# Performance work log

Hardware: AMD Instinct MI355X
Metric: run time of the kernel (lower is better)

Reference implementation:

```python
import jax, jax.numpy as jnp
import numpy as np

DIM = 768
HEADS = 12
SCALE = DIM ** -0.5  # NOTE: module scales by full dim, not head dim


def setup_inputs() -> dict:
    key = jax.random.key(0)
    ks = jax.random.split(key, 5)
    B, N, C = 8, 1024, DIM
    x = jax.random.normal(ks[0], (B, N, C), dtype=jnp.float32)
    W_qkv = jax.random.normal(ks[1], (C, 3 * C), dtype=jnp.float32) * (C ** -0.5)
    b_qkv = jnp.zeros((3 * C,), dtype=jnp.float32)
    W_out = jax.random.normal(ks[2], (C, C), dtype=jnp.float32) * (C ** -0.5)
    b_out = jnp.zeros((C,), dtype=jnp.float32)
    return {"x": x, "W_qkv": W_qkv, "b_qkv": b_qkv, "W_out": W_out, "b_out": b_out}


def reference(x, W_qkv, b_qkv, W_out, b_out) -> jnp.ndarray:
    B, N, C = x.shape
    H, D = HEADS, C // HEADS
    qkv = x @ W_qkv + b_qkv                       # [B, N, 3C]
    q, k, v = jnp.split(qkv, 3, axis=-1)
    # [B, N, C] -> [B, H, N, D]
    q = q.reshape(B, N, H, D).transpose(0, 2, 1, 3)
    k = k.reshape(B, N, H, D).transpose(0, 2, 1, 3)
    v = v.reshape(B, N, H, D).transpose(0, 2, 1, 3)
    attn = jnp.einsum("bhnd,bhmd->bhnm", q, k) * SCALE
    attn = jax.nn.softmax(attn, axis=-1)
    out = jnp.einsum("bhnm,bhmd->bhnd", attn, v)   # [B, H, N, D]
    out = out.transpose(0, 2, 1, 3).reshape(B, N, C)
    return out @ W_out + b_out
```

## Files before the change

kernel.cpp:

```cpp
#include <hip/hip_runtime.h>
#include <hip/hip_bf16.h>

typedef __attribute__((ext_vector_type(4))) float f32x4;
typedef __attribute__((ext_vector_type(4))) unsigned u32x4;
typedef __attribute__((ext_vector_type(8))) short bf16x8;

#define QSCALE  (0.03608439182435161f * 1.44269504088896f)

__device__ __forceinline__ unsigned short f2bf(float f) {
    union { float f; unsigned u; } v; v.f = f;
    return (unsigned short)((v.u + 0x7FFFu + ((v.u >> 16) & 1u)) >> 16);
}

__device__ __forceinline__ float fast_exp2(float x) {
#if __has_builtin(__builtin_amdgcn_exp2f)
    return __builtin_amdgcn_exp2f(x);
#else
    return exp2f(x);
#endif
}

__device__ __forceinline__ void gload_lds16(const void* g, void* l) {
    __builtin_amdgcn_global_load_lds(
        (const __attribute__((address_space(1))) unsigned int*)g,
        (__attribute__((address_space(3))) unsigned int*)l, 16, 0, 0);
}

__global__ __launch_bounds__(256) void prep_kernel(
    const float* __restrict__ X, unsigned short* __restrict__ Xb,
    const float* __restrict__ Wqkv, unsigned short* __restrict__ WqkvT,
    const float* __restrict__ Wout, unsigned short* __restrict__ WoutT)
{
    __shared__ unsigned short T[64][68];
    const int bid = blockIdx.x, t = threadIdx.x;

    if (bid < 3072) {
        const int i = bid * 256 + t;
        f32x4 a = *(const f32x4*)(X + (size_t)i * 8);
        f32x4 b = *(const f32x4*)(X + (size_t)i * 8 + 4);
        bf16x8 w;
#pragma unroll
        for (int j = 0; j < 4; ++j) { w[j] = (short)f2bf(a[j]); w[4 + j] = (short)f2bf(b[j]); }
        *(bf16x8*)(Xb + (size_t)i * 8) = w;
        return;
    }

    const float* W; unsigned short* WT; int C, bx, by;
    if (bid < 3504) { W = Wqkv; WT = WqkvT; C = 2304; const int x = bid - 3072; bx = x % 36; by = x / 36; }
    else            { W = Wout; WT = WoutT; C = 768;  const int x = bid - 3504; bx = x % 12; by = x / 12; }
    const int R = 768;
    const int r0 = by * 64, c0 = bx * 64;
    {
        const int lr = t >> 4, lc = (t & 15) * 4;
#pragma unroll
        for (int p = 0; p < 4; ++p) {
            const float* s = W + (size_t)(r0 + lr + p * 16) * C + c0 + lc;
            f32x4 v = *(const f32x4*)s;
            unsigned short* d = &T[lr + p * 16][lc];
            d[0] = f2bf(v[0]); d[1] = f2bf(v[1]); d[2] = f2bf(v[2]); d[3] = f2bf(v[3]);
        }
    }
    __syncthreads();
    {
        const int oc = t >> 3, j0 = (t & 7) * 8;
#pragma unroll
        for (int p = 0; p < 2; ++p) {
            const int c = oc + p * 32;
            bf16x8 v;
#pragma unroll
            for (int j = 0; j < 8; ++j) v[j] = (short)T[j0 + j][c];
            *(bf16x8*)(WT + (size_t)(c0 + c) * R + r0 + j0) = v;
        }
    }
}

__global__ __launch_bounds__(256) void qkv_gemm_kernel(
    const unsigned short* __restrict__ Xb, const unsigned short* __restrict__ WT,
    const float* __restrict__ bias,
    unsigned short* __restrict__ Qw, unsigned short* __restrict__ Kw,
    unsigned short* __restrict__ VTw)
{
    __shared__ unsigned short SMEM[64 * 136 + 64];
    unsigned short* Alds = SMEM;
    unsigned short* Blds = SMEM + 128 * 32;

    const int t = threadIdx.x;
    const int lane = t & 63, wave = t >> 6;
    const int l15 = lane & 15, l4 = lane >> 4;
    const int m0 = blockIdx.x * 128, n0 = blockIdx.y * 64;
    const int wr = wave >> 1, wc = wave & 1;

    f32x4 acc[4][2];
#pragma unroll
    for (int m = 0; m < 4; ++m)
#pragma unroll
        for (int n = 0; n < 2; ++n) acc[m][n] = (f32x4){0.f, 0.f, 0.f, 0.f};

    for (int k0 = 0; k0 < 768; k0 += 32) {
#pragma unroll
        for (int c = 0; c < 2; ++c) {
            const int o = wave * 1024 + lane * 16 + c * 4096;
            const int row = o >> 6, cb = o & 63;
            gload_lds16((const char*)(Xb + (size_t)(m0 + row) * 768 + k0) + cb,
                        (char*)Alds + wave * 1024 + c * 4096);
        }
        {
            const int o = t * 16;
            const int row = o >> 6, cb = o & 63;
            gload_lds16((const char*)(WT + (size_t)(n0 + row) * 768 + k0) + cb,
                        (char*)Blds + o);
        }
        __syncthreads();
        bf16x8 af[4], bfr[2];
#pragma unroll
        for (int m = 0; m < 4; ++m)
            af[m] = *(const bf16x8*)((const char*)Alds + (wr * 64 + m * 16 + l15) * 64 + l4 * 16);
#pragma unroll
        for (int n = 0; n < 2; ++n)
            bfr[n] = *(const bf16x8*)((const char*)Blds + (wc * 32 + n * 16 + l15) * 64 + l4 * 16);
#pragma unroll
        for (int m = 0; m < 4; ++m)
#pragma unroll
            for (int n = 0; n < 2; ++n)
                acc[m][n] = __builtin_amdgcn_mfma_f32_16x16x32_bf16(af[m], bfr[n], acc[m][n], 0, 0, 0);
        __syncthreads();
    }

    const int b = m0 >> 10, ntok0 = m0 & 1023;
    if (n0 < 1536) {
        const int which = n0 / 768;
        const int h = (n0 - which * 768) >> 6;
#pragma unroll
        for (int n = 0; n < 2; ++n) {
            const int dd = wc * 32 + n * 16 + l15;
            const float bv = bias[n0 + dd];
#pragma unroll
            for (int m = 0; m < 4; ++m)
#pragma unroll
                for (int r = 0; r < 4; ++r) {
                    const int ntl = wr * 64 + m * 16 + l4 * 4 + r;
                    float val = acc[m][n][r] + bv;
                    if (which == 0) val *= QSCALE;
                    SMEM[ntl * 68 + dd] = f2bf(val);
                }
        }
        __syncthreads();
        {
            unsigned short* dst = (which == 0 ? Qw : Kw)
                + ((size_t)(b * 12 + h) * 1024 + ntok0) * 64;
            const int k8 = (t & 7) * 8;
#pragma unroll
            for (int pass = 0; pass < 4; ++pass) {
                const int row = pass * 32 + (t >> 3);
                *(bf16x8*)&dst[(size_t)row * 64 + k8] =
                    *(const bf16x8*)&SMEM[row * 68 + k8];
            }
        }
    } else {
        const int h = (n0 - 1536) >> 6;
#pragma unroll
        for (int n = 0; n < 2; ++n) {
            const int cloc = wc * 32 + n * 16 + l15;
            const float bv = bias[n0 + cloc];
#pragma unroll
            for (int m = 0; m < 4; ++m)
#pragma unroll
                for (int r = 0; r < 4; ++r) {
                    const int ntl = wr * 64 + m * 16 + l4 * 4 + r;
                    SMEM[cloc * 136 + ntl] = f2bf(acc[m][n][r] + bv);
                }
        }
        __syncthreads();
        {
            const int sub = t & 15;
#pragma unroll
            for (int rep = 0; rep < 4; ++rep) {
                const int cll = rep * 16 + (t >> 4);
                const size_t rb = ((size_t)(b * 12 + h) * 64 + cll) * 1024 + ntok0 + sub * 8;
                *(bf16x8*)&VTw[rb] = *(const bf16x8*)&SMEM[cll * 136 + sub * 8];
            }
        }
    }
}

__global__ __launch_bounds__(256) void attn_kernel(
    const unsigned short* __restrict__ Qw, const unsigned short* __restrict__ Kw,
    const unsigned short* __restrict__ VTw, unsigned short* __restrict__ A2)
{
    __shared__ unsigned short Klds[2 * 64 * 64];
    __shared__ unsigned short Vlds[2 * 64 * 64];
    __shared__ float Flds[4 * 2 * 16];

    const int t = threadIdx.x, lane = t & 63, wave = t >> 6;
    const int l15 = lane & 15, l4 = lane >> 4;
    const int wg = (blockIdx.x & 7) * 96 + (blockIdx.x >> 3);
    const int qt = wg & 7, bh = wg >> 3;
    const int q0 = qt * 128;

    const size_t kvbase = (size_t)bh * 1024 * 64;
    const size_t vtbase = (size_t)bh * 64 * 1024;

    bf16x8 qf[2][2];
#pragma unroll
    for (int qs = 0; qs < 2; ++qs) {
        const unsigned short* qptr = Qw + kvbase + (size_t)(q0 + qs * 64 + wave * 16 + l15) * 64;
        qf[qs][0] = *(const bf16x8*)((const char*)qptr + l4 * 16);
        qf[qs][1] = *(const bf16x8*)((const char*)qptr + 64 + l4 * 16);
    }

    f32x4 oacc[2][4];
#pragma unroll
    for (int qs = 0; qs < 2; ++qs)
#pragma unroll
        for (int d = 0; d < 4; ++d) oacc[qs][d] = (f32x4){0.f, 0.f, 0.f, 0.f};
    float m_run[2] = {-1e30f, -1e30f}, l_run[2] = {0.f, 0.f};

    auto STAGE = [&](int kt, int bufi) {
        const int kv0 = kt * 64;
        char* kb = (char*)Klds + bufi * 8192;
        char* vb = (char*)Vlds + bufi * 8192;
#pragma unroll
        for (int c = 0; c < 2; ++c) {
            const int oo = wave * 1024 + lane * 16 + c * 4096;
            const int R = oo >> 7, w = oo & 127;
            const int sw = w ^ ((R & 7) << 4);
            const int kvs = (R & 0x23) | ((R & 0x0C) << 1) | ((R & 0x10) >> 2);
            gload_lds16((const char*)(Kw + kvbase + (size_t)(kv0 + kvs) * 64) + sw,
                        kb + wave * 1024 + c * 4096);
            gload_lds16((const char*)(VTw + vtbase + (size_t)R * 1024 + kv0) + sw,
                        vb + wave * 1024 + c * 4096);
        }
    };

    STAGE(0, 0);
    for (int kt = 0; kt < 16; ++kt) {
        const int cur = kt & 1;
        if (kt < 15) {
            STAGE(kt + 1, cur ^ 1);
            asm volatile("s_waitcnt vmcnt(4)" ::: "memory");
        } else {
            asm volatile("s_waitcnt vmcnt(0)" ::: "memory");
        }
        __builtin_amdgcn_s_barrier();
        __builtin_amdgcn_sched_barrier(0);
        const char* kb = (const char*)Klds + cur * 8192;
        const char* vb = (const char*)Vlds + cur * 8192;

#pragma unroll
        for (int qs = 0; qs < 2; ++qs) {
            f32x4 sacc[4];
#pragma unroll
            for (int i = 0; i < 4; ++i) sacc[i] = (f32x4){0.f, 0.f, 0.f, 0.f};
            __builtin_amdgcn_s_setprio(1);
#pragma unroll
            for (int ks = 0; ks < 2; ++ks) {
                const bf16x8 qq = qf[qs][ks];
#pragma unroll
                for (int kvf = 0; kvf < 4; ++kvf) {
                    const int row = kvf * 16 + l15;
                    int addr = row * 128 + ks * 64 + l4 * 16;
                    addr ^= (row & 7) << 4;
                    const bf16x8 kf = *(const bf16x8*)(kb + addr);
                    sacc[kvf] = __builtin_amdgcn_mfma_f32_16x16x32_bf16(kf, qq, sacc[kvf], 0, 0, 0);
                }
            }
            __builtin_amdgcn_s_setprio(0);

            float p[16];
            float tmax = -1e30f;
#pragma unroll
            for (int i = 0; i < 4; ++i)
#pragma unroll
                for (int r = 0; r < 4; ++r) {
                    p[i * 4 + r] = sacc[i][r];
                    tmax = fmaxf(tmax, sacc[i][r]);
                }
            tmax = fmaxf(tmax, __shfl_xor(tmax, 16));
            tmax = fmaxf(tmax, __shfl_xor(tmax, 32));

            if (!__all(tmax - m_run[qs] <= 8.f)) {
                const float mnew = fmaxf(m_run[qs], tmax);
                const float alpha = fast_exp2(m_run[qs] - mnew);
                m_run[qs] = mnew;
                if (lane < 16) Flds[wave * 32 + qs * 16 + lane] = alpha;
                const f32x4 av = *(const f32x4*)(&Flds[wave * 32 + qs * 16 + l4 * 4]);
#pragma unroll
                for (int d = 0; d < 4; ++d)
#pragma unroll
                    for (int r = 0; r < 4; ++r) oacc[qs][d][r] *= av[r];
                l_run[qs] *= alpha;
            }

            float tsum = 0.f;
#pragma unroll
            for (int i = 0; i < 16; ++i) { p[i] = fast_exp2(p[i] - m_run[qs]); tsum += p[i]; }
            tsum += __shfl_xor(tsum, 16);
            tsum += __shfl_xor(tsum, 32);
            l_run[qs] += tsum;

            bf16x8 paf[2];
#pragma unroll
            for (int ks = 0; ks < 2; ++ks) {
                union { u32x4 u; bf16x8 h; } cv;
#pragma unroll
                for (int j2 = 0; j2 < 4; ++j2)
                    asm("v_cvt_pk_bf16_f32 %0, %1, %2"
                        : "=v"(cv.u[j2]) : "v"(p[ks * 8 + 2 * j2]), "v"(p[ks * 8 + 2 * j2 + 1]));
                paf[ks] = cv.h;
            }

            __builtin_amdgcn_s_setprio(1);
#pragma unroll
            for (int ks = 0; ks < 2; ++ks) {
#pragma unroll
                for (int df = 0; df < 4; ++df) {
                    const int d = df * 16 + l15;
                    int addr = d * 128 + ks * 64 + l4 * 16;
                    addr ^= (d & 7) << 4;
                    const bf16x8 vf = *(const bf16x8*)(vb + addr);
                    oacc[qs][df] = __builtin_amdgcn_mfma_f32_16x16x32_bf16(paf[ks], vf, oacc[qs][df], 0, 0, 0);
                }
            }
            __builtin_amdgcn_s_setprio(0);
        }
        __builtin_amdgcn_s_barrier();
    }

    const int b = bh / 12, h = bh - b * 12;
#pragma unroll
    for (int qs = 0; qs < 2; ++qs) {
        if (lane < 16) Flds[wave * 32 + qs * 16 + lane] = 1.f / l_run[qs];
        const f32x4 inv = *(const f32x4*)(&Flds[wave * 32 + qs * 16 + l4 * 4]);
#pragma unroll
        for (int df = 0; df < 4; ++df) {
#pragma unroll
            for (int r = 0; r < 4; ++r) {
                const int row = b * 1024 + q0 + qs * 64 + wave * 16 + l4 * 4 + r;
                const int col = h * 64 + df * 16 + l15;
                A2[(size_t)row * 768 + col] = f2bf(oacc[qs][df][r] * inv[r]);
            }
        }
    }
}

__global__ __launch_bounds__(256) void out_gemm_kernel(
    const unsigned short* __restrict__ A2, const unsigned short* __restrict__ WT,
    const float* __restrict__ bias, float* __restrict__ Out)
{
    __shared__ unsigned short Alds[128 * 32];
    __shared__ unsigned short Blds[64 * 32];

    const int t = threadIdx.x;
    const int lane = t & 63, wave = t >> 6;
    const int l15 = lane & 15, l4 = lane >> 4;
    const int m0 = blockIdx.x * 128, n0 = blockIdx.y * 64;
    const int wr = wave >> 1, wc = wave & 1;

    f32x4 acc[4][2];
#pragma unroll
    for (int m = 0; m < 4; ++m)
#pragma unroll
        for (int n = 0; n < 2; ++n) acc[m][n] = (f32x4){0.f, 0.f, 0.f, 0.f};

    for (int k0 = 0; k0 < 768; k0 += 32) {
#pragma unroll
        for (int c = 0; c < 2; ++c) {
            const int o = wave * 1024 + lane * 16 + c * 4096;
            const int row = o >> 6, cb = o & 63;
            gload_lds16((const char*)(A2 + (size_t)(m0 + row) * 768 + k0) + cb,
                        (char*)Alds + wave * 1024 + c * 4096);
        }
        {
            const int o = t * 16;
            const int row = o >> 6, cb = o & 63;
            gload_lds16((const char*)(WT + (size_t)(n0 + row) * 768 + k0) + cb,
                        (char*)Blds + o);
        }
        __syncthreads();
        bf16x8 af[4], bfr[2];
#pragma unroll
        for (int m = 0; m < 4; ++m)
            af[m] = *(const bf16x8*)((const char*)Alds + (wr * 64 + m * 16 + l15) * 64 + l4 * 16);
#pragma unroll
        for (int n = 0; n < 2; ++n)
            bfr[n] = *(const bf16x8*)((const char*)Blds + (wc * 32 + n * 16 + l15) * 64 + l4 * 16);
#pragma unroll
        for (int m = 0; m < 4; ++m)
#pragma unroll
            for (int n = 0; n < 2; ++n)
                acc[m][n] = __builtin_amdgcn_mfma_f32_16x16x32_bf16(af[m], bfr[n], acc[m][n], 0, 0, 0);
        __syncthreads();
    }

#pragma unroll
    for (int n = 0; n < 2; ++n) {
        const int col = n0 + wc * 32 + n * 16 + l15;
        const float bv = bias[col];
#pragma unroll
        for (int m = 0; m < 4; ++m)
#pragma unroll
            for (int r = 0; r < 4; ++r) {
                const int row = m0 + wr * 64 + m * 16 + l4 * 4 + r;
                Out[(size_t)row * 768 + col] = acc[m][n][r] + bv;
            }
    }
}

extern "C" void kernel_launch(void* const* d_in, const int* in_sizes, int n_in,
                              void* d_out, int out_size, void* d_ws, size_t ws_size,
                              hipStream_t stream) {
    const float* X    = (const float*)d_in[0];
    const float* Wqkv = (const float*)d_in[1];
    const float* bqkv = (const float*)d_in[2];
    const float* Wout = (const float*)d_in[3];
    const float* bout = (const float*)d_in[4];
    float* Out = (float*)d_out;

    const size_t nq = (size_t)96 * 1024 * 64;
    unsigned short* XbA2  = (unsigned short*)d_ws;
    unsigned short* Qw    = XbA2 + nq;
    unsigned short* Kw    = Qw + nq;
    unsigned short* VTw   = Kw + nq;
    unsigned short* WqkvT = VTw + nq;
    unsigned short* WoutT = WqkvT + (size_t)2304 * 768;

    hipLaunchKernelGGL(prep_kernel, dim3(3648), dim3(256), 0, stream,
                       X, XbA2, Wqkv, WqkvT, Wout, WoutT);
    hipLaunchKernelGGL(qkv_gemm_kernel, dim3(64, 36), dim3(256), 0, stream,
                       XbA2, WqkvT, bqkv, Qw, Kw, VTw);
    hipLaunchKernelGGL(attn_kernel, dim3(768), dim3(256), 0, stream,
                       Qw, Kw, VTw, XbA2);
    hipLaunchKernelGGL(out_gemm_kernel, dim3(64, 12), dim3(256), 0, stream,
                       XbA2, WoutT, bout, Out);
}
```

Before: 124.8 us.

## Triple-buffer QKV GEMM LDS staging with single barrier per k-step

Restructures the QKV projection GEMM main loop to use three LDS buffers, prefetching the next k-slice via global_load_lds while computing the current one. Uses a partial vmcnt wait and one barrier per iteration instead of two syncthreads, and raises wave priority around the MFMA block. This is meant to hide global load latency behind matrix work, at the cost of more LDS per block, which may reduce occupancy.

```diff
diff --git a/kernel.cpp b/kernel.cpp
--- a/kernel.cpp
+++ b/kernel.cpp
@@ -80,9 +80,7 @@
     unsigned short* __restrict__ Qw, unsigned short* __restrict__ Kw,
     unsigned short* __restrict__ VTw)
 {
-    __shared__ unsigned short SMEM[64 * 136 + 64];
-    unsigned short* Alds = SMEM;
-    unsigned short* Blds = SMEM + 128 * 32;
+    __shared__ unsigned short SMEM[3 * 6144];
 
     const int t = threadIdx.x;
     const int lane = t & 63, wave = t >> 6;
@@ -96,35 +94,55 @@
 #pragma unroll
         for (int n = 0; n < 2; ++n) acc[m][n] = (f32x4){0.f, 0.f, 0.f, 0.f};
 
-    for (int k0 = 0; k0 < 768; k0 += 32) {
+    auto STAGE = [&](int k0, int bufi) {
+        char* base = (char*)SMEM + bufi * 12288;
 #pragma unroll
         for (int c = 0; c < 2; ++c) {
             const int o = wave * 1024 + lane * 16 + c * 4096;
             const int row = o >> 6, cb = o & 63;
             gload_lds16((const char*)(Xb + (size_t)(m0 + row) * 768 + k0) + cb,
-                        (char*)Alds + wave * 1024 + c * 4096);
+                        base + wave * 1024 + c * 4096);
         }
         {
             const int o = t * 16;
             const int row = o >> 6, cb = o & 63;
             gload_lds16((const char*)(WT + (size_t)(n0 + row) * 768 + k0) + cb,
-                        (char*)Blds + o);
-        }
-        __syncthreads();
-        bf16x8 af[4], bfr[2];
-#pragma unroll
-        for (int m = 0; m < 4; ++m)
-            af[m] = *(const bf16x8*)((const char*)Alds + (wr * 64 + m * 16 + l15) * 64 + l4 * 16);
-#pragma unroll
-        for (int n = 0; n < 2; ++n)
-            bfr[n] = *(const bf16x8*)((const char*)Blds + (wc * 32 + n * 16 + l15) * 64 + l4 * 16);
-#pragma unroll
-        for (int m = 0; m < 4; ++m)
+                        base + 8192 + o);
+        }
+    };
+
+    STAGE(0, 0);
+    for (int g = 0; g < 8; ++g) {
+#pragma unroll
+        for (int p = 0; p < 3; ++p) {
+            const int k = g * 3 + p;
+            if (k < 23) {
+                STAGE((k + 1) * 32, (p + 1) % 3);
+                asm volatile("s_waitcnt vmcnt(3)" ::: "memory");
+            } else {
+                asm volatile("s_waitcnt vmcnt(0)" ::: "memory");
+            }
+            __builtin_amdgcn_s_barrier();
+            __builtin_amdgcn_sched_barrier(0);
+
+            const char* base = (const char*)SMEM + p * 12288;
+            bf16x8 af[4], bfr[2];
+#pragma unroll
+            for (int m = 0; m < 4; ++m)
+                af[m] = *(const bf16x8*)(base + (wr * 64 + m * 16 + l15) * 64 + l4 * 16);
 #pragma unroll
             for (int n = 0; n < 2; ++n)
-                acc[m][n] = __builtin_amdgcn_mfma_f32_16x16x32_bf16(af[m], bfr[n], acc[m][n], 0, 0, 0);
-        __syncthreads();
-    }
+                bfr[n] = *(const bf16x8*)(base + 8192 + (wc * 32 + n * 16 + l15) * 64 + l4 * 16);
+            __builtin_amdgcn_s_setprio(1);
+#pragma unroll
+            for (int m = 0; m < 4; ++m)
+#pragma unroll
+                for (int n = 0; n < 2; ++n)
+                    acc[m][n] = __builtin_amdgcn_mfma_f32_16x16x32_bf16(af[m], bfr[n], acc[m][n], 0, 0, 0);
+            __builtin_amdgcn_s_setprio(0);
+        }
+    }
+    __syncthreads();
 
     const int b = m0 >> 10, ntok0 = m0 & 1023;
     if (n0 < 1536) {
```

Result: no change. 122.6 us (-1.7%).
